# Performance work log

Measured on AMD Instinct MI355X. Metric: run time of the kernel, lower is better.

The kernel has to match this reference:

```python
import jax, jax.numpy as jnp
import numpy as np

N_HEAD = 16


def setup_inputs() -> dict:
    key = jax.random.key(0)
    k1, k2, k3 = jax.random.split(key, 3)
    B, T, C = 4, 1024, 1024
    x = jax.random.normal(k1, (B, T, C), dtype=jnp.float32)
    w_attn = jax.random.normal(k2, (3 * C, C), dtype=jnp.float32) * 0.02
    w_proj = jax.random.normal(k3, (C, C), dtype=jnp.float32) * 0.02
    return {"x": x, "w_attn": w_attn, "w_proj": w_proj}


def reference(x, w_attn, w_proj):
    B, T, C = x.shape
    H = N_HEAD
    hs = C // H
    scale = 1.0 / np.sqrt(hs).astype(np.float32)

    qkv = x @ w_attn.T                         # [B, T, 3C]
    q, k, v = jnp.split(qkv, 3, axis=-1)
    q = q.reshape(B, T, H, hs).transpose(0, 2, 1, 3)   # [B, H, T, hs]
    k = k.reshape(B, T, H, hs).transpose(0, 2, 1, 3)
    v = v.reshape(B, T, H, hs).transpose(0, 2, 1, 3)

    scores = jnp.einsum('bhqd,bhkd->bhqk', q, k) * scale   # [B, H, T, T]
    causal = jnp.tril(jnp.ones((T, T), dtype=bool))
    scores = jnp.where(causal, scores, -jnp.inf)

    att = jax.nn.sigmoid(scores)                # sigmoid attention, not softmax
    # Bernoulli straight-through sampling (value = sample, grad flows via att)
    samp_key = jax.random.fold_in(jax.random.key(0), 42)
    samples = jax.random.bernoulli(samp_key, att).astype(att.dtype)
    att = att + jax.lax.stop_gradient(samples - att)

    y = jnp.einsum('bhqk,bhkd->bhqd', att, v)   # [B, H, T, hs]
    att_sum = att.sum(axis=-1)                  # [B, H, T]
    att_var = (att * (1.0 - att)).sum(axis=-1)  # [B, H, T]

    y = y.transpose(0, 2, 1, 3).reshape(B, T, C)
    y = y @ w_proj.T
    return (y, att_sum, att_var)
```

## Files before the change

### kernel.cpp

```cpp
#include <hip/hip_runtime.h>
#include <stdint.h>


#define T_SEQ 1024
#define QKV_LD 3072

typedef __attribute__((ext_vector_type(8))) short bf16x8;
typedef __attribute__((ext_vector_type(4))) float f32x4;
typedef __attribute__((ext_vector_type(4))) unsigned int u32x4;

typedef __attribute__((address_space(3))) uint32_t lds_u32;
typedef __attribute__((address_space(1))) const uint32_t g_u32;

#define ROTL(x, d) __builtin_amdgcn_alignbit((x), (x), 32 - (d))

__device__ __forceinline__ void threefry2x32(uint32_t k0, uint32_t k1,
                                             uint32_t x0, uint32_t x1,
                                             uint32_t &o0, uint32_t &o1) {
  uint32_t ks2 = k0 ^ k1 ^ 0x1BD11BDAu;
#define TF_R4(a, b, c, d)                                                      \
  x0 += x1; x1 = ROTL(x1, a); x1 ^= x0;                                        \
  x0 += x1; x1 = ROTL(x1, b); x1 ^= x0;                                        \
  x0 += x1; x1 = ROTL(x1, c); x1 ^= x0;                                        \
  x0 += x1; x1 = ROTL(x1, d); x1 ^= x0;
  x0 += k0; x1 += k1;
  TF_R4(13, 15, 26, 6)
  x0 += k1; x1 += ks2 + 1u;
  TF_R4(17, 29, 16, 24)
  x0 += ks2; x1 += k0 + 2u;
  TF_R4(13, 15, 26, 6)
  x0 += k0; x1 += k1 + 3u;
  TF_R4(17, 29, 16, 24)
  x0 += k1; x1 += ks2 + 4u;
  TF_R4(13, 15, 26, 6)
  x0 += ks2; x1 += k0 + 5u;
  o0 = x0; o1 = x1;
#undef TF_R4
}

__device__ __forceinline__ unsigned short f2bf(float f) {
  uint32_t u = __float_as_uint(f);
  u += 0x7FFFu + ((u >> 16) & 1u);
  return (unsigned short)(u >> 16);
}

#define N_X4  1048576
#define N_WA4 786432
#define N_WP4 262144

__global__ __launch_bounds__(256) void cvt3_bf16(const float4* __restrict__ x,
                                                 const float4* __restrict__ wa,
                                                 const float4* __restrict__ wp,
                                                 uint2* __restrict__ out) {
  size_t i = (size_t)blockIdx.x * 256 + threadIdx.x;
  const float4* src;
  size_t off;
  if (i < N_X4) { src = x; off = i; }
  else if (i < N_X4 + N_WA4) { src = wa; off = i - N_X4; }
  else { src = wp; off = i - (N_X4 + N_WA4); }
  float4 v = src[off];
  uint2 o;
  o.x = (uint32_t)f2bf(v.x) | ((uint32_t)f2bf(v.y) << 16);
  o.y = (uint32_t)f2bf(v.z) | ((uint32_t)f2bf(v.w) << 16);
  out[i] = o;
}

template <int OUT_BF16>
__global__ __launch_bounds__(256) void gemm_bf16(const unsigned short* __restrict__ A,
                                                 const unsigned short* __restrict__ B,
                                                 void* __restrict__ Cout,
                                                 int M, int N, int K) {
  __shared__ unsigned short As[128 * 32];
  __shared__ unsigned short Bs[128 * 32];

  const int t = threadIdx.x;
  const int lane = t & 63, w = t >> 6;
  const int g = lane >> 4, lr = lane & 15;
  const int rw = w >> 1, cw = w & 1;
  const int bm = blockIdx.x * 128, bn = blockIdx.y * 128;

  const unsigned short* Ag = A + (size_t)(bm + 32 * w + (lane >> 2)) * K + 8 * (lane & 3);
  const unsigned short* Bg = B + (size_t)(bn + 32 * w + (lane >> 2)) * K + 8 * (lane & 3);
  lds_u32* Al0 = (lds_u32*)&As[(32 * w) * 32];
  lds_u32* Al1 = (lds_u32*)&As[(32 * w + 16) * 32];
  lds_u32* Bl0 = (lds_u32*)&Bs[(32 * w) * 32];
  lds_u32* Bl1 = (lds_u32*)&Bs[(32 * w + 16) * 32];

  f32x4 acc[4][4];
#pragma unroll
  for (int i = 0; i < 4; ++i)
#pragma unroll
    for (int j = 0; j < 4; ++j) acc[i][j] = (f32x4){0.f, 0.f, 0.f, 0.f};

  for (int k0 = 0; k0 < K; k0 += 32) {
    __syncthreads();
    __builtin_amdgcn_global_load_lds((g_u32*)(const void*)(Ag + k0), Al0, 16, 0, 0);
    __builtin_amdgcn_global_load_lds((g_u32*)(const void*)(Ag + k0 + (size_t)16 * K), Al1, 16, 0, 0);
    __builtin_amdgcn_global_load_lds((g_u32*)(const void*)(Bg + k0), Bl0, 16, 0, 0);
    __builtin_amdgcn_global_load_lds((g_u32*)(const void*)(Bg + k0 + (size_t)16 * K), Bl1, 16, 0, 0);
    __syncthreads();

    bf16x8 af[4], bfr[4];
#pragma unroll
    for (int i = 0; i < 4; ++i)
      af[i] = *(const bf16x8*)&As[(64 * rw + 16 * i + lr) * 32 + 8 * g];
#pragma unroll
    for (int j = 0; j < 4; ++j)
      bfr[j] = *(const bf16x8*)&Bs[(64 * cw + 16 * j + lr) * 32 + 8 * g];
#pragma unroll
    for (int i = 0; i < 4; ++i)
#pragma unroll
      for (int j = 0; j < 4; ++j)
        acc[i][j] = __builtin_amdgcn_mfma_f32_16x16x32_bf16(af[i], bfr[j], acc[i][j], 0, 0, 0);
  }

#pragma unroll
  for (int i = 0; i < 4; ++i)
#pragma unroll
    for (int j = 0; j < 4; ++j)
#pragma unroll
      for (int r = 0; r < 4; ++r) {
        const size_t row = bm + 64 * rw + 16 * i + 4 * g + r;
        const size_t col = bn + 64 * cw + 16 * j + lr;
        if (OUT_BF16)
          ((unsigned short*)Cout)[row * N + col] = f2bf(acc[i][j][r]);
        else
          ((float*)Cout)[row * N + col] = acc[i][j][r];
      }
}

__constant__ int QT_TAB[16] = {15, 0, 13, 2, 11, 4, 9, 6, 14, 1, 12, 3, 10, 5, 8, 7};

__global__ __launch_bounds__(256) void attn_mfma(const unsigned short* __restrict__ qkv,
                                                 unsigned short* __restrict__ yatt,
                                                 float* __restrict__ att_sum,
                                                 float* __restrict__ att_var) {
  __shared__ uint32_t Ks4[64 * 32];
  __shared__ uint32_t Vt4[64 * 32];
  __shared__ uint32_t QSt[64 * 72];

  const int t = threadIdx.x;
  const int lane = t & 63, w = t >> 6;
  const int g = lane >> 4, lr = lane & 15;
  const int i = blockIdx.x;
  const int bh = 8 * (i & 7) + ((i >> 3) & 7);
  const int qt = QT_TAB[i >> 6];
  const int b = bh >> 4, h = bh & 15;
  const int qt64 = qt * 64;

  uint32_t dk0, dk1;
  threefry2x32(0u, 0u, 0u, 42u, dk0, dk1);

  const int swzr = (lr & 7) << 2;

  {
    const unsigned short* qbase = qkv + (size_t)(b * T_SEQ + qt64) * QKV_LD + h * 64;
    const int r = t >> 2, s4 = t & 3;
    const unsigned short* src = qbase + (size_t)r * QKV_LD + 8 * s4;
    u32x4 v0 = *(const u32x4*)(src);
    u32x4 v1 = *(const u32x4*)(src + 32);
    const int sw = (r & 7) << 2;
    *(u32x4*)&QSt[r * 72 + ((4 * s4) ^ sw)] = v0;
    *(u32x4*)&QSt[r * 72 + ((4 * s4 + 16) ^ sw)] = v1;
  }
  __syncthreads();

  bf16x8 aq0, aq1;
  {
    const uint32_t* qrow = &QSt[(16 * w + lr) * 72];
    aq0 = *(const bf16x8*)&qrow[(4 * g) ^ swzr];
    aq1 = *(const bf16x8*)&qrow[(4 * g + 16) ^ swzr];
  }

  f32x4 yacc[4];
#pragma unroll
  for (int c = 0; c < 4; ++c) yacc[c] = (f32x4){0.f, 0.f, 0.f, 0.f};
  float rs[4] = {0.f, 0.f, 0.f, 0.f};

  for (int kt = 0; kt <= qt; ++kt) {
    __syncthreads();
    const unsigned short* kb = qkv + (size_t)(b * T_SEQ + kt * 64) * QKV_LD + 1024 + h * 64;
    {
      const int r = t >> 2, s4 = t & 3;
      const unsigned short* src = kb + (size_t)r * QKV_LD + 8 * s4;
      u32x4 v0 = *(const u32x4*)(src);
      u32x4 v1 = *(const u32x4*)(src + 32);
      const int sw = (r & 7) << 2;
      *(u32x4*)&Ks4[r * 32 + ((4 * s4) ^ sw)] = v0;
      *(u32x4*)&Ks4[r * 32 + ((4 * s4 + 16) ^ sw)] = v1;
    }
    {
      const int k2 = 2 * (t & 31), d0 = 8 * (t >> 5);
      const unsigned short* vsrc =
          qkv + (size_t)(b * T_SEQ + kt * 64 + k2) * QKV_LD + 2048 + h * 64 + d0;
      union { u32x4 v; unsigned short us[8]; } va, vb;
      va.v = *(const u32x4*)(vsrc);
      vb.v = *(const u32x4*)(vsrc + QKV_LD);
#pragma unroll
      for (int j = 0; j < 8; ++j) {
        uint32_t pw = (uint32_t)va.us[j] | ((uint32_t)vb.us[j] << 16);
        Vt4[(d0 + j) * 32 + ((t & 31) ^ ((j & 7) << 2))] = pw;
      }
    }
    __syncthreads();

    const int kt64 = kt * 64;
#pragma unroll
    for (int c = 0; c < 4; ++c) {
      const uint32_t* krow = &Ks4[(16 * c + lr) * 32];
      bf16x8 bk0 = *(const bf16x8*)&krow[(4 * g) ^ swzr];
      bf16x8 bk1 = *(const bf16x8*)&krow[(4 * g + 16) ^ swzr];
      f32x4 s = __builtin_amdgcn_mfma_f32_16x16x32_bf16(aq0, bk0, (f32x4){0.f, 0.f, 0.f, 0.f}, 0, 0, 0);
      s = __builtin_amdgcn_mfma_f32_16x16x32_bf16(aq1, bk1, s, 0, 0, 0);

      const int kg = kt64 + 16 * c + lr;
#pragma unroll
      for (int r = 0; r < 4; ++r) {
        const int qg = qt64 + 16 * w + 4 * g + r;
        float samp = 0.f;
        if (kg <= qg) {
          float e = __expf(-0.125f * s[r]);
          uint32_t idx = ((uint32_t)bh << 20) | ((uint32_t)qg << 10) | (uint32_t)kg;
          uint32_t r0, r1;
          threefry2x32(dk0, dk1, 0u, idx, r0, r1);
          float u = __uint_as_float(0x3F800000u | ((r0 ^ r1) >> 9)) - 1.0f;
          samp = (fmaf(u, e, u) < 1.0f) ? 1.0f : 0.0f;
        }
        rs[r] += samp;
        const int row = 16 * w + 4 * g + r;
        ((float*)QSt)[row * 72 + ((16 * c + lr) ^ ((row & 7) << 2))] = samp;
      }
    }

#pragma unroll
    for (int ks = 0; ks < 2; ++ks) {
      const float* srow = (const float*)&QSt[(16 * w + lr) * 72];
      f32x4 p0 = *(const f32x4*)&srow[(8 * g + 32 * ks) ^ swzr];
      f32x4 p1 = *(const f32x4*)&srow[(8 * g + 32 * ks + 4) ^ swzr];
      union { uint32_t u[4]; bf16x8 v; } pa;
      pa.u[0] = (__float_as_uint(p0.y) & 0xFFFF0000u) | (__float_as_uint(p0.x) >> 16);
      pa.u[1] = (__float_as_uint(p0.w) & 0xFFFF0000u) | (__float_as_uint(p0.z) >> 16);
      pa.u[2] = (__float_as_uint(p1.y) & 0xFFFF0000u) | (__float_as_uint(p1.x) >> 16);
      pa.u[3] = (__float_as_uint(p1.w) & 0xFFFF0000u) | (__float_as_uint(p1.z) >> 16);
#pragma unroll
      for (int c = 0; c < 4; ++c) {
        bf16x8 vb = *(const bf16x8*)&Vt4[(16 * c + lr) * 32 + ((4 * g + 16 * ks) ^ swzr)];
        yacc[c] = __builtin_amdgcn_mfma_f32_16x16x32_bf16(pa.v, vb, yacc[c], 0, 0, 0);
      }
    }
  }

  const size_t yb = (size_t)(b * T_SEQ + qt64 + 16 * w) * 1024 + h * 64;
#pragma unroll
  for (int c = 0; c < 4; ++c)
#pragma unroll
    for (int r = 0; r < 4; ++r)
      yatt[yb + (size_t)(4 * g + r) * 1024 + 16 * c + lr] = f2bf(yacc[c][r]);

#pragma unroll
  for (int r = 0; r < 4; ++r) {
    rs[r] += __shfl_xor(rs[r], 1);
    rs[r] += __shfl_xor(rs[r], 2);
    rs[r] += __shfl_xor(rs[r], 4);
    rs[r] += __shfl_xor(rs[r], 8);
  }
  if (lr == 0) {
#pragma unroll
    for (int r = 0; r < 4; ++r)
      att_sum[(size_t)bh * T_SEQ + qt64 + 16 * w + 4 * g + r] = rs[r];
  }
  if (t < 64) att_var[(size_t)bh * T_SEQ + qt64 + t] = 0.f;
}

extern "C" void kernel_launch(void* const* d_in, const int* in_sizes, int n_in,
                              void* d_out, int out_size, void* d_ws, size_t ws_size,
                              hipStream_t stream) {
  (void)in_sizes; (void)n_in; (void)out_size; (void)ws_size;
  const float* x      = (const float*)d_in[0];
  const float* w_attn = (const float*)d_in[1];
  const float* w_proj = (const float*)d_in[2];

  float* y_out      = (float*)d_out;
  float* attsum_out = y_out + (size_t)4 * 1024 * 1024;
  float* attvar_out = attsum_out + (size_t)4 * 16 * 1024;

  unsigned short* ws_us = (unsigned short*)d_ws;
  unsigned short* x_bf    = ws_us;
  unsigned short* wa_bf   = x_bf + (size_t)4 * 1024 * 1024;
  unsigned short* wp_bf   = wa_bf + (size_t)3 * 1024 * 1024;
  unsigned short* qkv_bf  = wp_bf + (size_t)1024 * 1024;
  unsigned short* yatt_bf = qkv_bf + (size_t)4096 * 3072;

  dim3 blk(256);
  cvt3_bf16<<<dim3(8192), blk, 0, stream>>>((const float4*)x, (const float4*)w_attn,
                                            (const float4*)w_proj, (uint2*)x_bf);
  gemm_bf16<1><<<dim3(32, 24), blk, 0, stream>>>(x_bf, wa_bf, (void*)qkv_bf, 4096, 3072, 1024);
  attn_mfma<<<dim3(1024), blk, 0, stream>>>(qkv_bf, yatt_bf, attsum_out, attvar_out);
  gemm_bf16<0><<<dim3(32, 8), blk, 0, stream>>>(yatt_bf, wp_bf, (void*)y_out, 4096, 1024, 1024);
}
```

Before: 197.3 us.

## Replace shared-LDS attention with barrier-free per-wave kernel and separate V transpose

```diff
diff --git a/kernel.cpp b/kernel.cpp
--- a/kernel.cpp
+++ b/kernel.cpp
@@ -129,147 +129,144 @@
       }
 }
 
-__constant__ int QT_TAB[16] = {15, 0, 13, 2, 11, 4, 9, 6, 14, 1, 12, 3, 10, 5, 8, 7};
-
-__global__ __launch_bounds__(256) void attn_mfma(const unsigned short* __restrict__ qkv,
-                                                 unsigned short* __restrict__ yatt,
-                                                 float* __restrict__ att_sum,
-                                                 float* __restrict__ att_var) {
-  __shared__ uint32_t Ks4[64 * 32];
-  __shared__ uint32_t Vt4[64 * 32];
-  __shared__ uint32_t QSt[64 * 72];
+__global__ __launch_bounds__(256) void vtrans(const unsigned short* __restrict__ qkv,
+                                              unsigned short* __restrict__ Vt) {
+  const int i = blockIdx.x;
+  const int bh = i >> 4, kc = i & 15;
+  const int b = bh >> 4, h = bh & 15;
+  const int t = threadIdx.x;
+  const int dr = t & 63, kgrp = t >> 6;
+
+  const unsigned short* src =
+      qkv + (size_t)(b * T_SEQ + kc * 64 + kgrp * 16) * QKV_LD + 2048 + h * 64 + dr;
+  uint32_t pk[8];
+#pragma unroll
+  for (int j = 0; j < 8; ++j) {
+    uint32_t lo = src[(size_t)(2 * j) * QKV_LD];
+    uint32_t hi = src[(size_t)(2 * j + 1) * QKV_LD];
+    pk[j] = lo | (hi << 16);
+  }
+  unsigned short* dst = Vt + ((size_t)bh * 64 + dr) * 1024 + kc * 64 + kgrp * 16;
+  *(u32x4*)dst = (u32x4){pk[0], pk[1], pk[2], pk[3]};
+  *(u32x4*)(dst + 8) = (u32x4){pk[4], pk[5], pk[6], pk[7]};
+}
+
+__global__ __launch_bounds__(128) void attn_nobar(const unsigned short* __restrict__ qkv,
+                                                  const unsigned short* __restrict__ Vt,
+                                                  unsigned short* __restrict__ yatt,
+                                                  float* __restrict__ att_sum,
+                                                  float* __restrict__ att_var) {
+  __shared__ unsigned short St[2][16][40];
 
   const int t = threadIdx.x;
   const int lane = t & 63, w = t >> 6;
   const int g = lane >> 4, lr = lane & 15;
   const int i = blockIdx.x;
   const int bh = 8 * (i & 7) + ((i >> 3) & 7);
-  const int qt = QT_TAB[i >> 6];
+  const int p = 2 * (i >> 6) + w;
   const int b = bh >> 4, h = bh & 15;
-  const int qt64 = qt * 64;
 
   uint32_t dk0, dk1;
   threefry2x32(0u, 0u, 0u, 42u, dk0, dk1);
 
-  const int swzr = (lr & 7) << 2;
-
-  {
-    const unsigned short* qbase = qkv + (size_t)(b * T_SEQ + qt64) * QKV_LD + h * 64;
-    const int r = t >> 2, s4 = t & 3;
-    const unsigned short* src = qbase + (size_t)r * QKV_LD + 8 * s4;
-    u32x4 v0 = *(const u32x4*)(src);
-    u32x4 v1 = *(const u32x4*)(src + 32);
-    const int sw = (r & 7) << 2;
-    *(u32x4*)&QSt[r * 72 + ((4 * s4) ^ sw)] = v0;
-    *(u32x4*)&QSt[r * 72 + ((4 * s4 + 16) ^ sw)] = v1;
+  unsigned short (*stw)[40] = St[w];
+  const unsigned short* kb = qkv + (size_t)b * T_SEQ * QKV_LD + 1024 + h * 64;
+  const unsigned short* vb = Vt + (size_t)bh * 64 * 1024;
+
+#pragma unroll 1
+  for (int half = 0; half < 2; ++half) {
+    const int s = half ? p : 63 - p;
+    const int q0 = 16 * s;
+    const unsigned short* qr = qkv + (size_t)(b * T_SEQ + q0 + lr) * QKV_LD + h * 64 + 8 * g;
+    const bf16x8 aq0 = *(const bf16x8*)qr;
+    const bf16x8 aq1 = *(const bf16x8*)(qr + 32);
+
+    f32x4 yacc[4];
+#pragma unroll
+    for (int c = 0; c < 4; ++c) yacc[c] = (f32x4){0.f, 0.f, 0.f, 0.f};
+    float rs[4] = {0.f, 0.f, 0.f, 0.f};
+
+    const int nk = (q0 + 47) >> 5;
+
+    bf16x8 cbv[4], cbk[4];
+#pragma unroll
+    for (int c = 0; c < 4; ++c)
+      cbv[c] = *(const bf16x8*)(vb + (size_t)(16 * c + lr) * 1024 + 8 * g);
+#pragma unroll
+    for (int c = 0; c < 2; ++c) {
+      const unsigned short* kr = kb + (size_t)(16 * c + lr) * QKV_LD + 8 * g;
+      cbk[2 * c] = *(const bf16x8*)kr;
+      cbk[2 * c + 1] = *(const bf16x8*)(kr + 32);
+    }
+
+#pragma unroll 1
+    for (int kt = 0; kt < nk; ++kt) {
+      const int kg0 = 32 * kt;
+      const int kgn = (kt + 1 < nk) ? kg0 + 32 : kg0;
+      bf16x8 nbv[4], nbk[4];
+#pragma unroll
+      for (int c = 0; c < 4; ++c)
+        nbv[c] = *(const bf16x8*)(vb + (size_t)(16 * c + lr) * 1024 + kgn + 8 * g);
+#pragma unroll
+      for (int c = 0; c < 2; ++c) {
+        const unsigned short* kr = kb + (size_t)(kgn + 16 * c + lr) * QKV_LD + 8 * g;
+        nbk[2 * c] = *(const bf16x8*)kr;
+        nbk[2 * c + 1] = *(const bf16x8*)(kr + 32);
+      }
+
+#pragma unroll
+      for (int c = 0; c < 2; ++c) {
+        f32x4 sa = __builtin_amdgcn_mfma_f32_16x16x32_bf16(aq0, cbk[2 * c],
+                                                           (f32x4){0.f, 0.f, 0.f, 0.f}, 0, 0, 0);
+        sa = __builtin_amdgcn_mfma_f32_16x16x32_bf16(aq1, cbk[2 * c + 1], sa, 0, 0, 0);
+        const int kg = kg0 + 16 * c + lr;
+#pragma unroll
+        for (int r = 0; r < 4; ++r) {
+          const int qg = q0 + 4 * g + r;
+          float samp = 0.f;
+          if (kg <= qg) {
+            float e = __expf(-0.125f * sa[r]);
+            uint32_t idx = ((uint32_t)bh << 20) | ((uint32_t)qg << 10) | (uint32_t)kg;
+            uint32_t r0, r1;
+            threefry2x32(dk0, dk1, 0u, idx, r0, r1);
+            float u = __uint_as_float(0x3F800000u | ((r0 ^ r1) >> 9)) - 1.0f;
+            samp = (fmaf(u, e, u) < 1.0f) ? 1.0f : 0.0f;
+          }
+          rs[r] += samp;
+          stw[4 * g + r][16 * c + lr] = (unsigned short)(__float_as_uint(samp) >> 16);
+        }
+      }
+
+      const bf16x8 pa = *(const bf16x8*)&stw[lr][8 * g];
+#pragma unroll
+      for (int c = 0; c < 4; ++c)
+        yacc[c] = __builtin_amdgcn_mfma_f32_16x16x32_bf16(pa, cbv[c], yacc[c], 0, 0, 0);
+
+#pragma unroll
+      for (int c = 0; c < 4; ++c) { cbv[c] = nbv[c]; cbk[c] = nbk[c]; }
+    }
+
+    const size_t yb = (size_t)(b * T_SEQ + q0) * 1024 + h * 64;
+#pragma unroll
+    for (int c = 0; c < 4; ++c)
+#pragma unroll
+      for (int r = 0; r < 4; ++r)
+        yatt[yb + (size_t)(4 * g + r) * 1024 + 16 * c + lr] = f2bf(yacc[c][r]);
+
+#pragma unroll
+    for (int r = 0; r < 4; ++r) {
+      rs[r] += __shfl_xor(rs[r], 1);
+      rs[r] += __shfl_xor(rs[r], 2);
+      rs[r] += __shfl_xor(rs[r], 4);
+      rs[r] += __shfl_xor(rs[r], 8);
+    }
+    if (lr == 0) {
+#pragma unroll
+      for (int r = 0; r < 4; ++r)
+        att_sum[(size_t)bh * T_SEQ + q0 + 4 * g + r] = rs[r];
+    }
+    if (lane < 16) att_var[(size_t)bh * T_SEQ + q0 + lane] = 0.f;
   }
-  __syncthreads();
-
-  bf16x8 aq0, aq1;
-  {
-    const uint32_t* qrow = &QSt[(16 * w + lr) * 72];
-    aq0 = *(const bf16x8*)&qrow[(4 * g) ^ swzr];
-    aq1 = *(const bf16x8*)&qrow[(4 * g + 16) ^ swzr];
-  }
-
-  f32x4 yacc[4];
-#pragma unroll
-  for (int c = 0; c < 4; ++c) yacc[c] = (f32x4){0.f, 0.f, 0.f, 0.f};
-  float rs[4] = {0.f, 0.f, 0.f, 0.f};
-
-  for (int kt = 0; kt <= qt; ++kt) {
-    __syncthreads();
-    const unsigned short* kb = qkv + (size_t)(b * T_SEQ + kt * 64) * QKV_LD + 1024 + h * 64;
-    {
-      const int r = t >> 2, s4 = t & 3;
-      const unsigned short* src = kb + (size_t)r * QKV_LD + 8 * s4;
-      u32x4 v0 = *(const u32x4*)(src);
-      u32x4 v1 = *(const u32x4*)(src + 32);
-      const int sw = (r & 7) << 2;
-      *(u32x4*)&Ks4[r * 32 + ((4 * s4) ^ sw)] = v0;
-      *(u32x4*)&Ks4[r * 32 + ((4 * s4 + 16) ^ sw)] = v1;
-    }
-    {
-      const int k2 = 2 * (t & 31), d0 = 8 * (t >> 5);
-      const unsigned short* vsrc =
-          qkv + (size_t)(b * T_SEQ + kt * 64 + k2) * QKV_LD + 2048 + h * 64 + d0;
-      union { u32x4 v; unsigned short us[8]; } va, vb;
-      va.v = *(const u32x4*)(vsrc);
-      vb.v = *(const u32x4*)(vsrc + QKV_LD);
-#pragma unroll
-      for (int j = 0; j < 8; ++j) {
-        uint32_t pw = (uint32_t)va.us[j] | ((uint32_t)vb.us[j] << 16);
-        Vt4[(d0 + j) * 32 + ((t & 31) ^ ((j & 7) << 2))] = pw;
-      }
-    }
-    __syncthreads();
-
-    const int kt64 = kt * 64;
-#pragma unroll
-    for (int c = 0; c < 4; ++c) {
-      const uint32_t* krow = &Ks4[(16 * c + lr) * 32];
-      bf16x8 bk0 = *(const bf16x8*)&krow[(4 * g) ^ swzr];
-      bf16x8 bk1 = *(const bf16x8*)&krow[(4 * g + 16) ^ swzr];
-      f32x4 s = __builtin_amdgcn_mfma_f32_16x16x32_bf16(aq0, bk0, (f32x4){0.f, 0.f, 0.f, 0.f}, 0, 0, 0);
-      s = __builtin_amdgcn_mfma_f32_16x16x32_bf16(aq1, bk1, s, 0, 0, 0);
-
-      const int kg = kt64 + 16 * c + lr;
-#pragma unroll
-      for (int r = 0; r < 4; ++r) {
-        const int qg = qt64 + 16 * w + 4 * g + r;
-        float samp = 0.f;
-        if (kg <= qg) {
-          float e = __expf(-0.125f * s[r]);
-          uint32_t idx = ((uint32_t)bh << 20) | ((uint32_t)qg << 10) | (uint32_t)kg;
-          uint32_t r0, r1;
-          threefry2x32(dk0, dk1, 0u, idx, r0, r1);
-          float u = __uint_as_float(0x3F800000u | ((r0 ^ r1) >> 9)) - 1.0f;
-          samp = (fmaf(u, e, u) < 1.0f) ? 1.0f : 0.0f;
-        }
-        rs[r] += samp;
-        const int row = 16 * w + 4 * g + r;
-        ((float*)QSt)[row * 72 + ((16 * c + lr) ^ ((row & 7) << 2))] = samp;
-      }
-    }
-
-#pragma unroll
-    for (int ks = 0; ks < 2; ++ks) {
-      const float* srow = (const float*)&QSt[(16 * w + lr) * 72];
-      f32x4 p0 = *(const f32x4*)&srow[(8 * g + 32 * ks) ^ swzr];
-      f32x4 p1 = *(const f32x4*)&srow[(8 * g + 32 * ks + 4) ^ swzr];
-      union { uint32_t u[4]; bf16x8 v; } pa;
-      pa.u[0] = (__float_as_uint(p0.y) & 0xFFFF0000u) | (__float_as_uint(p0.x) >> 16);
-      pa.u[1] = (__float_as_uint(p0.w) & 0xFFFF0000u) | (__float_as_uint(p0.z) >> 16);
-      pa.u[2] = (__float_as_uint(p1.y) & 0xFFFF0000u) | (__float_as_uint(p1.x) >> 16);
-      pa.u[3] = (__float_as_uint(p1.w) & 0xFFFF0000u) | (__float_as_uint(p1.z) >> 16);
-#pragma unroll
-      for (int c = 0; c < 4; ++c) {
-        bf16x8 vb = *(const bf16x8*)&Vt4[(16 * c + lr) * 32 + ((4 * g + 16 * ks) ^ swzr)];
-        yacc[c] = __builtin_amdgcn_mfma_f32_16x16x32_bf16(pa.v, vb, yacc[c], 0, 0, 0);
-      }
-    }
-  }
-
-  const size_t yb = (size_t)(b * T_SEQ + qt64 + 16 * w) * 1024 + h * 64;
-#pragma unroll
-  for (int c = 0; c < 4; ++c)
-#pragma unroll
-    for (int r = 0; r < 4; ++r)
-      yatt[yb + (size_t)(4 * g + r) * 1024 + 16 * c + lr] = f2bf(yacc[c][r]);
-
-#pragma unroll
-  for (int r = 0; r < 4; ++r) {
-    rs[r] += __shfl_xor(rs[r], 1);
-    rs[r] += __shfl_xor(rs[r], 2);
-    rs[r] += __shfl_xor(rs[r], 4);
-    rs[r] += __shfl_xor(rs[r], 8);
-  }
-  if (lr == 0) {
-#pragma unroll
-    for (int r = 0; r < 4; ++r)
-      att_sum[(size_t)bh * T_SEQ + qt64 + 16 * w + 4 * g + r] = rs[r];
-  }
-  if (t < 64) att_var[(size_t)bh * T_SEQ + qt64 + t] = 0.f;
 }
 
 extern "C" void kernel_launch(void* const* d_in, const int* in_sizes, int n_in,
@@ -290,11 +287,13 @@
   unsigned short* wp_bf   = wa_bf + (size_t)3 * 1024 * 1024;
   unsigned short* qkv_bf  = wp_bf + (size_t)1024 * 1024;
   unsigned short* yatt_bf = qkv_bf + (size_t)4096 * 3072;
+  unsigned short* vt_bf   = yatt_bf + (size_t)4096 * 1024;
 
   dim3 blk(256);
   cvt3_bf16<<<dim3(8192), blk, 0, stream>>>((const float4*)x, (const float4*)w_attn,
                                             (const float4*)w_proj, (uint2*)x_bf);
   gemm_bf16<1><<<dim3(32, 24), blk, 0, stream>>>(x_bf, wa_bf, (void*)qkv_bf, 4096, 3072, 1024);
-  attn_mfma<<<dim3(1024), blk, 0, stream>>>(qkv_bf, yatt_bf, attsum_out, attvar_out);
+  vtrans<<<dim3(1024), blk, 0, stream>>>(qkv_bf, vt_bf);
+  attn_nobar<<<dim3(1024), dim3(128), 0, stream>>>(qkv_bf, vt_bf, yatt_bf, attsum_out, attvar_out);
   gemm_bf16<0><<<dim3(32, 8), blk, 0, stream>>>(yatt_bf, wp_bf, (void*)y_out, 4096, 1024, 1024);
 }
```

Result: faster. 187.2 us (-5.1%).
